# Kernel tuning notes

Hardware: AMD Instinct MI355X
Metric: run time of the kernel (lower is better)

Reference implementation:

```python
import jax, jax.numpy as jnp
import numpy as np


def setup_inputs() -> dict:
    key = jax.random.key(0)
    k1, k2, k3, k4, k5 = jax.random.split(key, 5)
    return {
        "d1": jax.random.normal(k1, (2, 4096, 512), dtype=jnp.float32),
        "d2": jax.random.normal(k2, (2, 512, 4096), dtype=jnp.float32),
        "d3": jax.random.normal(k3, (2, 4096, 512), dtype=jnp.float32),
        "d4": jax.random.normal(k4, (512, 512), dtype=jnp.float32),
        "d5": jax.random.normal(k5, (1, 512), dtype=jnp.float32),
    }


def reference(d1, d2, d3, d4, d5):
    # attention core: scores = d1 @ d2 -> [2, 4096, 4096]
    scores = jnp.einsum('bsd,bdt->bst', d1, d2)
    attn = jax.nn.softmax(scores, axis=2)
    # weighted values: [2, 4096, 512]
    ctx = jnp.einsum('bst,btd->bsd', attn, d3)
    # flatten batch*seq and apply final projection with bias (addmm)
    x = ctx.reshape(8192, 512)
    return d5 + x @ d4  # d5 [1,512] broadcasts over rows
```

## Files before the change

kernel.cpp:

```cpp
#include <hip/hip_runtime.h>

typedef unsigned short u16;
typedef __attribute__((ext_vector_type(8))) short short8;
typedef __attribute__((ext_vector_type(4))) float f32x4;

#define MFMA16(a, b, c) __builtin_amdgcn_mfma_f32_16x16x32_bf16((a), (b), (c), 0, 0, 0)

constexpr int Bb = 2, Ss = 4096, Tt = 4096, Dd = 512;
constexpr int BM = 32, BN = 64, TP = 4;
constexpr int TPART = Tt / TP;
constexpr int TCH = TPART / BN;

constexpr size_t SZ_BF = (size_t)Bb * Tt * Dd * 2;
constexpr size_t O_D2TH = 0;
constexpr size_t O_D2TL = O_D2TH + SZ_BF;
constexpr size_t O_D3T  = O_D2TL + SZ_BF;
constexpr size_t O_D4T  = O_D3T + SZ_BF;
constexpr size_t O_CTX  = O_D4T + (size_t)512 * 512 * 2;
constexpr size_t O_OP   = O_CTX + SZ_BF;
constexpr size_t O_MP   = O_OP + (size_t)TP * SZ_BF;
constexpr size_t O_LP   = O_MP + (size_t)TP * Bb * Ss * 4;

__device__ __forceinline__ u16 f2bf(float x) {
  union { float f; unsigned u; } v; v.f = x;
  unsigned r = v.u + 0x7fffu + ((v.u >> 16) & 1u);
  return (u16)(r >> 16);
}
__device__ __forceinline__ float bf2f(u16 h) {
  union { unsigned u; float f; } v; v.u = ((unsigned)h) << 16;
  return v.f;
}

__global__ void transpose_split_kernel(const float* __restrict__ in,
                                       u16* __restrict__ outh,
                                       u16* __restrict__ outl,
                                       int R, int C) {
  __shared__ float tile[32][33];
  int b = blockIdx.z;
  const float* inb = in + (size_t)b * R * C;
  int x = blockIdx.x * 32 + threadIdx.x;
  int y0 = blockIdx.y * 32;
  for (int j = threadIdx.y; j < 32; j += 8)
    tile[j][threadIdx.x] = inb[(size_t)(y0 + j) * C + x];
  __syncthreads();
  size_t ob = (size_t)b * C * R;
  for (int j = threadIdx.y; j < 32; j += 8) {
    float v = tile[threadIdx.x][j];
    size_t oi = ob + (size_t)(blockIdx.x * 32 + j) * R + (y0 + threadIdx.x);
    u16 h = f2bf(v);
    outh[oi] = h;
    if (outl) outl[oi] = f2bf(v - bf2f(h));
  }
}

__global__ __launch_bounds__(128, 2)
void flash_part_kernel(const float* __restrict__ d1,
                       const u16* __restrict__ d2th,
                       const u16* __restrict__ d2tl,
                       const u16* __restrict__ d3t,
                       u16* __restrict__ opart,
                       float* __restrict__ mpart,
                       float* __restrict__ lpart) {
  __shared__ u16 qh[32 * 72], ql[32 * 72];
  __shared__ u16 kh[64 * 72], kl[64 * 72];
  __shared__ u16 ph[32 * 72];

  const int tid = threadIdx.x;
  const int wave = tid >> 6, lane = tid & 63, quad = lane >> 4, l15 = lane & 15;
  const int m0 = wave * 16;
  const int sblk = blockIdx.x, tp = blockIdx.y, b = blockIdx.z;
  const int s0 = sblk * BM;

  f32x4 o_acc[32];
#pragma unroll
  for (int i = 0; i < 32; i++) o_acc[i] = (f32x4){0.f, 0.f, 0.f, 0.f};
  float m_r[4] = {-INFINITY, -INFINITY, -INFINITY, -INFINITY};
  float l_r[4] = {0.f, 0.f, 0.f, 0.f};

  const float* q_base = d1 + ((size_t)b * Ss + s0) * Dd;
  const u16* kh_base = d2th + (size_t)b * Tt * Dd;
  const u16* kl_base = d2tl + (size_t)b * Tt * Dd;
  const u16* v_base  = d3t  + (size_t)b * Dd * Tt;

  const int qrow = tid >> 2, qcol = (tid & 3) * 16;
  const int krow = tid >> 1, kcol = (tid & 1) * 32;

  for (int tc = 0; tc < TCH; tc++) {
    const int t0 = tp * TPART + tc * BN;
    f32x4 s_acc[4];
#pragma unroll
    for (int nt = 0; nt < 4; nt++) s_acc[nt] = (f32x4){0.f, 0.f, 0.f, 0.f};

    for (int ds = 0; ds < 8; ds++) {
      const int d0 = ds * 64;
      __syncthreads();
      {
        const float* src = q_base + (size_t)qrow * Dd + d0 + qcol;
        u16* dh = &qh[qrow * 72 + qcol];
        u16* dl = &ql[qrow * 72 + qcol];
#pragma unroll
        for (int u = 0; u < 16; u += 4) {
          float4 v = *(const float4*)(src + u);
          ushort4 hh, ll;
          hh.x = f2bf(v.x); ll.x = f2bf(v.x - bf2f(hh.x));
          hh.y = f2bf(v.y); ll.y = f2bf(v.y - bf2f(hh.y));
          hh.z = f2bf(v.z); ll.z = f2bf(v.z - bf2f(hh.z));
          hh.w = f2bf(v.w); ll.w = f2bf(v.w - bf2f(hh.w));
          *(ushort4*)(dh + u) = hh;
          *(ushort4*)(dl + u) = ll;
        }
      }
      {
        const u16* sh = kh_base + (size_t)(t0 + krow) * Dd + d0 + kcol;
        const u16* sl = kl_base + (size_t)(t0 + krow) * Dd + d0 + kcol;
        u16* dh = &kh[krow * 72 + kcol];
        u16* dl = &kl[krow * 72 + kcol];
#pragma unroll
        for (int u = 0; u < 32; u += 8) {
          *(uint4*)(dh + u) = *(const uint4*)(sh + u);
          *(uint4*)(dl + u) = *(const uint4*)(sl + u);
        }
      }
      __syncthreads();
#pragma unroll
      for (int ks = 0; ks < 2; ks++) {
        const int kk = ks * 32 + quad * 8;
        short8 ah = *(const short8*)&qh[(m0 + l15) * 72 + kk];
        short8 al = *(const short8*)&ql[(m0 + l15) * 72 + kk];
#pragma unroll
        for (int nt = 0; nt < 4; nt++) {
          short8 bh = *(const short8*)&kh[(nt * 16 + l15) * 72 + kk];
          short8 bl = *(const short8*)&kl[(nt * 16 + l15) * 72 + kk];
          s_acc[nt] = MFMA16(ah, bh, s_acc[nt]);
          s_acc[nt] = MFMA16(al, bh, s_acc[nt]);
          s_acc[nt] = MFMA16(ah, bl, s_acc[nt]);
        }
      }
    }

    float alpha[4], psum[4];
#pragma unroll
    for (int r = 0; r < 4; r++) {
      float v = fmaxf(fmaxf(s_acc[0][r], s_acc[1][r]), fmaxf(s_acc[2][r], s_acc[3][r]));
      v = fmaxf(v, __shfl_xor(v, 1));
      v = fmaxf(v, __shfl_xor(v, 2));
      v = fmaxf(v, __shfl_xor(v, 4));
      v = fmaxf(v, __shfl_xor(v, 8));
      float mn = fmaxf(m_r[r], v);
      alpha[r] = __expf(m_r[r] - mn);
      m_r[r] = mn;
      psum[r] = 0.f;
    }
#pragma unroll
    for (int nt = 0; nt < 4; nt++) {
#pragma unroll
      for (int r = 0; r < 4; r++) {
        float p = __expf(s_acc[nt][r] - m_r[r]);
        psum[r] += p;
        ph[(m0 + quad * 4 + r) * 72 + nt * 16 + l15] = f2bf(p);
      }
    }
#pragma unroll
    for (int r = 0; r < 4; r++) {
      float v = psum[r];
      v += __shfl_xor(v, 1);
      v += __shfl_xor(v, 2);
      v += __shfl_xor(v, 4);
      v += __shfl_xor(v, 8);
      l_r[r] = l_r[r] * alpha[r] + v;
    }
#pragma unroll
    for (int j = 0; j < 32; j++) {
#pragma unroll
      for (int r = 0; r < 4; r++) o_acc[j][r] *= alpha[r];
    }

#pragma unroll
    for (int nc = 0; nc < 8; nc++) {
      __syncthreads();
      {
        const u16* sv = v_base + (size_t)(nc * 64 + krow) * Tt + t0 + kcol;
        u16* dv = &kh[krow * 72 + kcol];
#pragma unroll
        for (int u = 0; u < 32; u += 8) *(uint4*)(dv + u) = *(const uint4*)(sv + u);
      }
      __syncthreads();
#pragma unroll
      for (int ks = 0; ks < 2; ks++) {
        const int kk = ks * 32 + quad * 8;
        short8 ap = *(const short8*)&ph[(m0 + l15) * 72 + kk];
#pragma unroll
        for (int nt = 0; nt < 4; nt++) {
          short8 bv = *(const short8*)&kh[(nt * 16 + l15) * 72 + kk];
          o_acc[nc * 4 + nt] = MFMA16(ap, bv, o_acc[nc * 4 + nt]);
        }
      }
    }
  }

  const size_t obase = (((size_t)tp * Bb + b) * Ss + s0) * Dd;
#pragma unroll
  for (int j = 0; j < 32; j++) {
    const int col = (j >> 2) * 64 + (j & 3) * 16 + l15;
#pragma unroll
    for (int r = 0; r < 4; r++) {
      const int row = m0 + quad * 4 + r;
      opart[obase + (size_t)row * Dd + col] = f2bf(o_acc[j][r]);
    }
  }
  if (l15 == 0) {
    const size_t sbase = ((size_t)tp * Bb + b) * Ss + s0;
#pragma unroll
    for (int r = 0; r < 4; r++) {
      const int row = m0 + quad * 4 + r;
      mpart[sbase + row] = m_r[r];
      lpart[sbase + row] = l_r[r];
    }
  }
}

__global__ void combine_kernel(const u16* __restrict__ opart,
                               const float* __restrict__ mpart,
                               const float* __restrict__ lpart,
                               u16* __restrict__ ctx) {
  const int idx = blockIdx.x * blockDim.x + threadIdx.x;
  const int vpr = Dd / 8;
  const int row = idx / vpr;
  const int dv = (idx % vpr) * 8;
  float mv[TP], mM = -INFINITY;
#pragma unroll
  for (int p = 0; p < TP; p++) {
    mv[p] = mpart[(size_t)p * Bb * Ss + row];
    mM = fmaxf(mM, mv[p]);
  }
  float w[TP], denom = 0.f;
#pragma unroll
  for (int p = 0; p < TP; p++) {
    float e = __expf(mv[p] - mM);
    w[p] = e;
    denom += e * lpart[(size_t)p * Bb * Ss + row];
  }
  const float inv = 1.0f / denom;
  float acc[8];
#pragma unroll
  for (int e = 0; e < 8; e++) acc[e] = 0.f;
#pragma unroll
  for (int p = 0; p < TP; p++) {
    uint4 raw = *(const uint4*)&opart[(size_t)p * Bb * Ss * Dd + (size_t)row * Dd + dv];
    const u16* u = (const u16*)&raw;
#pragma unroll
    for (int e = 0; e < 8; e++) acc[e] += w[p] * bf2f(u[e]);
  }
  u16 outv[8];
#pragma unroll
  for (int e = 0; e < 8; e++) outv[e] = f2bf(acc[e] * inv);
  *(uint4*)&ctx[(size_t)row * Dd + dv] = *(const uint4*)outv;
}

__global__ __launch_bounds__(256, 2)
void proj_kernel(const u16* __restrict__ ctx,
                 const u16* __restrict__ d4t,
                 const float* __restrict__ d5,
                 float* __restrict__ out) {
  __shared__ u16 a_lds[128 * 40], b_lds[128 * 40];
  const int tid = threadIdx.x;
  const int wave = tid >> 6, lane = tid & 63, quad = lane >> 4, l15 = lane & 15;
  const int m0w = (wave & 1) * 64, n0w = (wave >> 1) * 64;
  const int bm = blockIdx.x, bn = blockIdx.y;
  f32x4 acc[4][4];
#pragma unroll
  for (int i = 0; i < 4; i++)
#pragma unroll
    for (int j = 0; j < 4; j++) acc[i][j] = (f32x4){0.f, 0.f, 0.f, 0.f};

  const int srow = tid >> 2, scol = (tid & 3) * 8;
  for (int kt = 0; kt < 16; kt++) {
    const int k0 = kt * 32;
    __syncthreads();
#pragma unroll
    for (int pass = 0; pass < 2; pass++) {
      const int row = srow + pass * 64;
      *(uint4*)&a_lds[row * 40 + scol] =
          *(const uint4*)&ctx[(size_t)(bm * 128 + row) * Dd + k0 + scol];
      *(uint4*)&b_lds[row * 40 + scol] =
          *(const uint4*)&d4t[(size_t)(bn * 128 + row) * Dd + k0 + scol];
    }
    __syncthreads();
    short8 af[4], bfr[4];
#pragma unroll
    for (int i = 0; i < 4; i++)
      af[i] = *(const short8*)&a_lds[(m0w + 16 * i + l15) * 40 + quad * 8];
#pragma unroll
    for (int j = 0; j < 4; j++)
      bfr[j] = *(const short8*)&b_lds[(n0w + 16 * j + l15) * 40 + quad * 8];
#pragma unroll
    for (int i = 0; i < 4; i++)
#pragma unroll
      for (int j = 0; j < 4; j++) acc[i][j] = MFMA16(af[i], bfr[j], acc[i][j]);
  }
#pragma unroll
  for (int j = 0; j < 4; j++) {
    const int colg = bn * 128 + n0w + 16 * j + l15;
    const float bias = d5[colg];
#pragma unroll
    for (int i = 0; i < 4; i++) {
#pragma unroll
      for (int r = 0; r < 4; r++) {
        const int rowg = bm * 128 + m0w + 16 * i + quad * 4 + r;
        out[(size_t)rowg * 512 + colg] = acc[i][j][r] + bias;
      }
    }
  }
}

extern "C" void kernel_launch(void* const* d_in, const int* in_sizes, int n_in,
                              void* d_out, int out_size, void* d_ws, size_t ws_size,
                              hipStream_t stream) {
  (void)in_sizes; (void)n_in; (void)out_size; (void)ws_size;
  const float* d1 = (const float*)d_in[0];
  const float* d2 = (const float*)d_in[1];
  const float* d3 = (const float*)d_in[2];
  const float* d4 = (const float*)d_in[3];
  const float* d5 = (const float*)d_in[4];
  float* out = (float*)d_out;
  char* ws = (char*)d_ws;

  u16* d2th = (u16*)(ws + O_D2TH);
  u16* d2tl = (u16*)(ws + O_D2TL);
  u16* d3t  = (u16*)(ws + O_D3T);
  u16* d4t  = (u16*)(ws + O_D4T);
  u16* ctx  = (u16*)(ws + O_CTX);
  u16* opart = (u16*)(ws + O_OP);
  float* mpart = (float*)(ws + O_MP);
  float* lpart = (float*)(ws + O_LP);

  transpose_split_kernel<<<dim3(128, 16, 2), dim3(32, 8), 0, stream>>>(d2, d2th, d2tl, 512, 4096);
  transpose_split_kernel<<<dim3(16, 128, 2), dim3(32, 8), 0, stream>>>(d3, d3t, nullptr, 4096, 512);
  transpose_split_kernel<<<dim3(16, 16, 1), dim3(32, 8), 0, stream>>>(d4, d4t, nullptr, 512, 512);

  flash_part_kernel<<<dim3(Ss / BM, TP, Bb), 128, 0, stream>>>(d1, d2th, d2tl, d3t,
                                                               opart, mpart, lpart);
  combine_kernel<<<(Bb * Ss * Dd / 8) / 256, 256, 0, stream>>>(opart, mpart, lpart, ctx);
  proj_kernel<<<dim3(64, 4), 256, 0, stream>>>(ctx, d4t, d5, out);
}
```

Baseline: 627.5 us.

## Pre-split Q to bf16 hi/lo, double query tile and widen K/V chunks

```diff
diff --git a/kernel.cpp b/kernel.cpp
--- a/kernel.cpp
+++ b/kernel.cpp
@@ -7,12 +7,14 @@
 #define MFMA16(a, b, c) __builtin_amdgcn_mfma_f32_16x16x32_bf16((a), (b), (c), 0, 0, 0)
 
 constexpr int Bb = 2, Ss = 4096, Tt = 4096, Dd = 512;
-constexpr int BM = 32, BN = 64, TP = 4;
+constexpr int BM = 64, BN = 64, TP = 4;
 constexpr int TPART = Tt / TP;
 constexpr int TCH = TPART / BN;
 
-constexpr size_t SZ_BF = (size_t)Bb * Tt * Dd * 2;
-constexpr size_t O_D2TH = 0;
+constexpr size_t SZ_BF = (size_t)Bb * Ss * Dd * 2;
+constexpr size_t O_QH  = 0;
+constexpr size_t O_QL  = O_QH + SZ_BF;
+constexpr size_t O_D2TH = O_QL + SZ_BF;
 constexpr size_t O_D2TL = O_D2TH + SZ_BF;
 constexpr size_t O_D3T  = O_D2TL + SZ_BF;
 constexpr size_t O_D4T  = O_D3T + SZ_BF;
@@ -29,6 +31,19 @@
 __device__ __forceinline__ float bf2f(u16 h) {
   union { unsigned u; float f; } v; v.u = ((unsigned)h) << 16;
   return v.f;
+}
+
+__global__ void cvt_split_kernel(const float* __restrict__ in,
+                                 u16* __restrict__ outh, u16* __restrict__ outl) {
+  const int i = blockIdx.x * 256 + threadIdx.x;
+  float4 v = ((const float4*)in)[i];
+  ushort4 hh, ll;
+  hh.x = f2bf(v.x); ll.x = f2bf(v.x - bf2f(hh.x));
+  hh.y = f2bf(v.y); ll.y = f2bf(v.y - bf2f(hh.y));
+  hh.z = f2bf(v.z); ll.z = f2bf(v.z - bf2f(hh.z));
+  hh.w = f2bf(v.w); ll.w = f2bf(v.w - bf2f(hh.w));
+  ((ushort4*)outh)[i] = hh;
+  ((ushort4*)outl)[i] = ll;
 }
 
 __global__ void transpose_split_kernel(const float* __restrict__ in,
@@ -53,23 +68,23 @@
   }
 }
 
-__global__ __launch_bounds__(128, 2)
-void flash_part_kernel(const float* __restrict__ d1,
+__global__ __launch_bounds__(256, 2)
+void flash_part_kernel(const u16* __restrict__ qh_g,
+                       const u16* __restrict__ ql_g,
                        const u16* __restrict__ d2th,
                        const u16* __restrict__ d2tl,
                        const u16* __restrict__ d3t,
                        u16* __restrict__ opart,
                        float* __restrict__ mpart,
                        float* __restrict__ lpart) {
-  __shared__ u16 qh[32 * 72], ql[32 * 72];
-  __shared__ u16 kh[64 * 72], kl[64 * 72];
-  __shared__ u16 ph[32 * 72];
+  __shared__ u16 kh[64 * 136], kl[64 * 136];
+  __shared__ u16 vb[128 * 72];
+  __shared__ u16 ph[64 * 72];
 
   const int tid = threadIdx.x;
   const int wave = tid >> 6, lane = tid & 63, quad = lane >> 4, l15 = lane & 15;
   const int m0 = wave * 16;
-  const int sblk = blockIdx.x, tp = blockIdx.y, b = blockIdx.z;
-  const int s0 = sblk * BM;
+  const int s0 = blockIdx.x * BM, tp = blockIdx.y, b = blockIdx.z;
 
   f32x4 o_acc[32];
 #pragma unroll
@@ -77,13 +92,14 @@
   float m_r[4] = {-INFINITY, -INFINITY, -INFINITY, -INFINITY};
   float l_r[4] = {0.f, 0.f, 0.f, 0.f};
 
-  const float* q_base = d1 + ((size_t)b * Ss + s0) * Dd;
-  const u16* kh_base = d2th + (size_t)b * Tt * Dd;
-  const u16* kl_base = d2tl + (size_t)b * Tt * Dd;
-  const u16* v_base  = d3t  + (size_t)b * Dd * Tt;
-
-  const int qrow = tid >> 2, qcol = (tid & 3) * 16;
-  const int krow = tid >> 1, kcol = (tid & 1) * 32;
+  const u16* qh_row = qh_g + ((size_t)b * Ss + s0 + m0 + l15) * Dd + quad * 8;
+  const u16* ql_row = ql_g + ((size_t)b * Ss + s0 + m0 + l15) * Dd + quad * 8;
+  const u16* kh_b = d2th + (size_t)b * Tt * Dd;
+  const u16* kl_b = d2tl + (size_t)b * Tt * Dd;
+  const u16* v_b  = d3t  + (size_t)b * Dd * Tt;
+
+  const int krow = tid >> 2, kcol = (tid & 3) * 32;
+  const int vrow = tid >> 1, vcol = (tid & 1) * 32;
 
   for (int tc = 0; tc < TCH; tc++) {
     const int t0 = tp * TPART + tc * BN;
@@ -91,30 +107,14 @@
 #pragma unroll
     for (int nt = 0; nt < 4; nt++) s_acc[nt] = (f32x4){0.f, 0.f, 0.f, 0.f};
 
-    for (int ds = 0; ds < 8; ds++) {
-      const int d0 = ds * 64;
+    for (int ds = 0; ds < 4; ds++) {
+      const int d0 = ds * 128;
       __syncthreads();
       {
-        const float* src = q_base + (size_t)qrow * Dd + d0 + qcol;
-        u16* dh = &qh[qrow * 72 + qcol];
-        u16* dl = &ql[qrow * 72 + qcol];
-#pragma unroll
-        for (int u = 0; u < 16; u += 4) {
-          float4 v = *(const float4*)(src + u);
-          ushort4 hh, ll;
-          hh.x = f2bf(v.x); ll.x = f2bf(v.x - bf2f(hh.x));
-          hh.y = f2bf(v.y); ll.y = f2bf(v.y - bf2f(hh.y));
-          hh.z = f2bf(v.z); ll.z = f2bf(v.z - bf2f(hh.z));
-          hh.w = f2bf(v.w); ll.w = f2bf(v.w - bf2f(hh.w));
-          *(ushort4*)(dh + u) = hh;
-          *(ushort4*)(dl + u) = ll;
-        }
-      }
-      {
-        const u16* sh = kh_base + (size_t)(t0 + krow) * Dd + d0 + kcol;
-        const u16* sl = kl_base + (size_t)(t0 + krow) * Dd + d0 + kcol;
-        u16* dh = &kh[krow * 72 + kcol];
-        u16* dl = &kl[krow * 72 + kcol];
+        const u16* sh = kh_b + (size_t)(t0 + krow) * Dd + d0 + kcol;
+        const u16* sl = kl_b + (size_t)(t0 + krow) * Dd + d0 + kcol;
+        u16* dh = &kh[krow * 136 + kcol];
+        u16* dl = &kl[krow * 136 + kcol];
 #pragma unroll
         for (int u = 0; u < 32; u += 8) {
           *(uint4*)(dh + u) = *(const uint4*)(sh + u);
@@ -122,18 +122,22 @@
         }
       }
       __syncthreads();
-#pragma unroll
-      for (int ks = 0; ks < 2; ks++) {
+      short8 ah[4], al[4];
+#pragma unroll
+      for (int ks = 0; ks < 4; ks++) {
+        ah[ks] = *(const short8*)(qh_row + d0 + ks * 32);
+        al[ks] = *(const short8*)(ql_row + d0 + ks * 32);
+      }
+#pragma unroll
+      for (int ks = 0; ks < 4; ks++) {
         const int kk = ks * 32 + quad * 8;
-        short8 ah = *(const short8*)&qh[(m0 + l15) * 72 + kk];
-        short8 al = *(const short8*)&ql[(m0 + l15) * 72 + kk];
 #pragma unroll
         for (int nt = 0; nt < 4; nt++) {
-          short8 bh = *(const short8*)&kh[(nt * 16 + l15) * 72 + kk];
-          short8 bl = *(const short8*)&kl[(nt * 16 + l15) * 72 + kk];
-          s_acc[nt] = MFMA16(ah, bh, s_acc[nt]);
-          s_acc[nt] = MFMA16(al, bh, s_acc[nt]);
-          s_acc[nt] = MFMA16(ah, bl, s_acc[nt]);
+          short8 bh = *(const short8*)&kh[(nt * 16 + l15) * 136 + kk];
+          short8 bl = *(const short8*)&kl[(nt * 16 + l15) * 136 + kk];
+          s_acc[nt] = MFMA16(ah[ks], bh, s_acc[nt]);
+          s_acc[nt] = MFMA16(al[ks], bh, s_acc[nt]);
+          s_acc[nt] = MFMA16(ah[ks], bl, s_acc[nt]);
         }
       }
     }
@@ -176,11 +180,11 @@
     }
 
 #pragma unroll
-    for (int nc = 0; nc < 8; nc++) {
+    for (int nc = 0; nc < 4; nc++) {
       __syncthreads();
       {
-        const u16* sv = v_base + (size_t)(nc * 64 + krow) * Tt + t0 + kcol;
-        u16* dv = &kh[krow * 72 + kcol];
+        const u16* sv = v_b + (size_t)(nc * 128 + vrow) * Tt + t0 + vcol;
+        u16* dv = &vb[vrow * 72 + vcol];
 #pragma unroll
         for (int u = 0; u < 32; u += 8) *(uint4*)(dv + u) = *(const uint4*)(sv + u);
       }
@@ -190,9 +194,9 @@
         const int kk = ks * 32 + quad * 8;
         short8 ap = *(const short8*)&ph[(m0 + l15) * 72 + kk];
 #pragma unroll
-        for (int nt = 0; nt < 4; nt++) {
-          short8 bv = *(const short8*)&kh[(nt * 16 + l15) * 72 + kk];
-          o_acc[nc * 4 + nt] = MFMA16(ap, bv, o_acc[nc * 4 + nt]);
+        for (int nt = 0; nt < 8; nt++) {
+          short8 bv = *(const short8*)&vb[(nt * 16 + l15) * 72 + kk];
+          o_acc[nc * 8 + nt] = MFMA16(ap, bv, o_acc[nc * 8 + nt]);
         }
       }
     }
@@ -201,7 +205,7 @@
   const size_t obase = (((size_t)tp * Bb + b) * Ss + s0) * Dd;
 #pragma unroll
   for (int j = 0; j < 32; j++) {
-    const int col = (j >> 2) * 64 + (j & 3) * 16 + l15;
+    const int col = (j >> 3) * 128 + (j & 7) * 16 + l15;
 #pragma unroll
     for (int r = 0; r < 4; r++) {
       const int row = m0 + quad * 4 + r;
@@ -325,6 +329,8 @@
   float* out = (float*)d_out;
   char* ws = (char*)d_ws;
 
+  u16* qh_g = (u16*)(ws + O_QH);
+  u16* ql_g = (u16*)(ws + O_QL);
   u16* d2th = (u16*)(ws + O_D2TH);
   u16* d2tl = (u16*)(ws + O_D2TL);
   u16* d3t  = (u16*)(ws + O_D3T);
@@ -334,11 +340,12 @@
   float* mpart = (float*)(ws + O_MP);
   float* lpart = (float*)(ws + O_LP);
 
+  cvt_split_kernel<<<(Bb * Ss * Dd / 4) / 256, 256, 0, stream>>>(d1, qh_g, ql_g);
   transpose_split_kernel<<<dim3(128, 16, 2), dim3(32, 8), 0, stream>>>(d2, d2th, d2tl, 512, 4096);
   transpose_split_kernel<<<dim3(16, 128, 2), dim3(32, 8), 0, stream>>>(d3, d3t, nullptr, 4096, 512);
   transpose_split_kernel<<<dim3(16, 16, 1), dim3(32, 8), 0, stream>>>(d4, d4t, nullptr, 512, 512);
 
-  flash_part_kernel<<<dim3(Ss / BM, TP, Bb), 128, 0, stream>>>(d1, d2th, d2tl, d3t,
+  flash_part_kernel<<<dim3(Ss / BM, TP, Bb), 256, 0, stream>>>(qh_g, ql_g, d2th, d2tl, d3t,
                                                                opart, mpart, lpart);
   combine_kernel<<<(Bb * Ss * Dd / 8) / 256, 256, 0, stream>>>(opart, mpart, lpart, ctx);
   proj_kernel<<<dim3(64, 4), 256, 0, stream>>>(ctx, d4t, d5, out);
```

Result: faster. 516.4 us (-17.7%).
